# Performance work log

Measured on AMD Instinct MI355X. Metric: run time of the kernel, lower is better.

## Reference

```python
import jax, jax.numpy as jnp
import numpy as np

N_NODES = 4096
N_EDGES = 131072
F_DIM = 16
H_DIM = 32

def _mlp_params(key, in_dim, hidden):
    ks = jax.random.split(key, 6)
    s1 = 1.0 / np.sqrt(in_dim); s2 = 1.0 / np.sqrt(hidden)
    return dict(
        W1=jax.random.uniform(ks[0], (in_dim, hidden), jnp.float32, -s1, s1),
        b1=jax.random.uniform(ks[1], (hidden,), jnp.float32, -s1, s1),
        W2=jax.random.uniform(ks[2], (hidden, hidden), jnp.float32, -s2, s2),
        b2=jax.random.uniform(ks[3], (hidden,), jnp.float32, -s2, s2),
        W3=jax.random.uniform(ks[4], (hidden, 1), jnp.float32, -s2, s2),
        b3=jax.random.uniform(ks[5], (1,), jnp.float32, -s2, s2),
    )

def _mlp(x, W1, b1, W2, b2, W3, b3):
    h = jax.nn.relu(x @ W1 + b1)
    h = jax.nn.relu(h @ W2 + b2)
    return (h @ W3 + b3)[..., 0]  # (E,)

def setup_inputs() -> dict:
    key = jax.random.key(0)
    k_ei, k_ef, k_s, k_p = jax.random.split(key, 4)
    edge_index = jax.random.randint(k_ei, (N_EDGES, 2), 0, N_NODES, dtype=jnp.int32)
    edge_feat = jax.random.normal(k_ef, (N_EDGES, F_DIM), dtype=jnp.float32)
    sh = _mlp_params(k_s, F_DIM, H_DIM)
    sp = _mlp_params(k_p, F_DIM, H_DIM)
    return dict(
        species_idx=0,
        edge_index=edge_index,
        edge_feat=edge_feat,
        num_nodes=N_NODES,
        sW1=sh['W1'], sb1=sh['b1'], sW2=sh['W2'], sb2=sh['b2'], sW3=sh['W3'], sb3=sh['b3'],
        pW1=sp['W1'], pb1=sp['b1'], pW2=sp['W2'], pb2=sp['b2'], pW3=sp['W3'], pb3=sp['b3'],
    )

def reference(species_idx, edge_index, edge_feat, num_nodes,
              sW1, sb1, sW2, sb2, sW3, sb3,
              pW1, pb1, pW2, pb2, pW3, pb3):
    # Edge logits: shared head + species head (species_idx selects the head;
    # here the selected head's params are passed directly).
    shared = _mlp(edge_feat, sW1, sb1, sW2, sb2, sW3, sb3)   # (E,)
    species = _mlp(edge_feat, pW1, pb1, pW2, pb2, pW3, pb3)  # (E,)
    resistance = jax.nn.softplus(shared + species) + 1e-4
    conductance = 1.0 / resistance
    i = edge_index[:, 0]
    j = edge_index[:, 1]
    # Scatter-assembled graph Laplacian (N x N)
    L = jnp.zeros((num_nodes, num_nodes), dtype=edge_feat.dtype)
    L = L.at[i, i].add(conductance)
    L = L.at[j, j].add(conductance)
    L = L.at[i, j].add(-conductance)
    L = L.at[j, i].add(-conductance)
    L_pinv = jnp.linalg.pinv(L)
    diag = jnp.diagonal(L_pinv)
    R = diag[:, None] + diag[None, :] - 2.0 * L_pinv
    return R, shared, species
```

## Files before the change

kernel.cpp:

```cpp
#include <hip/hip_runtime.h>
#include <hip/hip_bf16.h>


#define NN 4096
#define LDA 4096
#define NEDGE 131072
#define INVN (1.0f/4096.0f)

__device__ __forceinline__ float mlp_eval(const float* __restrict__ w,
                                          const float* __restrict__ x) {
  float h1[32], h2[32];
#pragma unroll
  for (int o = 0; o < 32; o += 4) {
    float4 s = *(const float4*)&w[512 + o];
#pragma unroll
    for (int i = 0; i < 16; ++i) {
      float4 wv = *(const float4*)&w[i * 32 + o];
      s.x = fmaf(x[i], wv.x, s.x); s.y = fmaf(x[i], wv.y, s.y);
      s.z = fmaf(x[i], wv.z, s.z); s.w = fmaf(x[i], wv.w, s.w);
    }
    h1[o] = fmaxf(s.x, 0.f); h1[o+1] = fmaxf(s.y, 0.f);
    h1[o+2] = fmaxf(s.z, 0.f); h1[o+3] = fmaxf(s.w, 0.f);
  }
#pragma unroll
  for (int o = 0; o < 32; o += 4) {
    float4 s = *(const float4*)&w[1568 + o];
#pragma unroll
    for (int i = 0; i < 32; ++i) {
      float4 wv = *(const float4*)&w[544 + i * 32 + o];
      s.x = fmaf(h1[i], wv.x, s.x); s.y = fmaf(h1[i], wv.y, s.y);
      s.z = fmaf(h1[i], wv.z, s.z); s.w = fmaf(h1[i], wv.w, s.w);
    }
    h2[o] = fmaxf(s.x, 0.f); h2[o+1] = fmaxf(s.y, 0.f);
    h2[o+2] = fmaxf(s.z, 0.f); h2[o+3] = fmaxf(s.w, 0.f);
  }
  float out = w[1632];
#pragma unroll
  for (int i = 0; i < 32; ++i) out = fmaf(h2[i], w[1600 + i], out);
  return out;
}

__global__ __launch_bounds__(256) void mlp_kernel(
    const float* __restrict__ ef,
    const float* __restrict__ sW1, const float* __restrict__ sb1,
    const float* __restrict__ sW2, const float* __restrict__ sb2,
    const float* __restrict__ sW3, const float* __restrict__ sb3,
    const float* __restrict__ pW1, const float* __restrict__ pb1,
    const float* __restrict__ pW2, const float* __restrict__ pb2,
    const float* __restrict__ pW3, const float* __restrict__ pb3,
    float* __restrict__ outS, float* __restrict__ outP,
    float* __restrict__ cond) {
  __shared__ float w[3328];
  int t = threadIdx.x;
  for (int i = t; i < 512; i += 256) { w[i] = sW1[i]; w[1664 + i] = pW1[i]; }
  for (int i = t; i < 1024; i += 256) { w[544 + i] = sW2[i]; w[1664 + 544 + i] = pW2[i]; }
  if (t < 32) {
    w[512 + t] = sb1[t]; w[1568 + t] = sb2[t]; w[1600 + t] = sW3[t];
    w[1664 + 512 + t] = pb1[t]; w[1664 + 1568 + t] = pb2[t]; w[1664 + 1600 + t] = pW3[t];
  }
  if (t == 0) { w[1632] = sb3[0]; w[1664 + 1632] = pb3[0]; }
  __syncthreads();
  int e = blockIdx.x * 256 + t;
  float x[16];
#pragma unroll
  for (int i = 0; i < 16; i += 4) {
    float4 v = *(const float4*)&ef[(size_t)e * 16 + i];
    x[i] = v.x; x[i+1] = v.y; x[i+2] = v.z; x[i+3] = v.w;
  }
  float s = mlp_eval(w, x);
  float p = mlp_eval(w + 1664, x);
  outS[e] = s; outP[e] = p;
  float z = s + p;
  float sp = fmaxf(z, 0.f) + log1pf(expf(-fabsf(z)));
  cond[e] = 1.0f / (sp + 1e-4f);
}

__global__ __launch_bounds__(256) void init_A(float* __restrict__ A) {
  size_t q = (size_t)blockIdx.x * 256 + threadIdx.x;
  *(float4*)&A[q * 4] = make_float4(INVN, INVN, INVN, INVN);
}

__global__ __launch_bounds__(256) void scatter_kernel(const int* __restrict__ ei,
                                                      const float* __restrict__ cond,
                                                      float* __restrict__ A) {
  int e = blockIdx.x * 256 + threadIdx.x;
  int i = ei[2 * e], j = ei[2 * e + 1];
  float c = cond[e];
  atomicAdd(&A[(size_t)i * (LDA + 1)], c);
  atomicAdd(&A[(size_t)j * (LDA + 1)], c);
  atomicAdd(&A[(size_t)i * LDA + j], -c);
  atomicAdd(&A[(size_t)j * LDA + i], -c);
}

__device__ __forceinline__ float rlane(float v, int l) {
  return __int_as_float(__builtin_amdgcn_readlane(__float_as_int(v), l));
}

__global__ __launch_bounds__(64) void potf2_wave(float* __restrict__ A, int k,
                                                 float* __restrict__ GinvAll) {
  float* blk = A + (size_t)k * 64 * (LDA + 1);
  const int lane = threadIdx.x;
  float a[64], x[64];
#pragma unroll
  for (int c = 0; c < 64; c += 4) {
    float4 v = *(const float4*)&blk[(size_t)lane * LDA + c];
    a[c] = v.x; a[c+1] = v.y; a[c+2] = v.z; a[c+3] = v.w;
    x[c]   = (c   == lane) ? 1.f : 0.f;
    x[c+1] = (c+1 == lane) ? 1.f : 0.f;
    x[c+2] = (c+2 == lane) ? 1.f : 0.f;
    x[c+3] = (c+3 == lane) ? 1.f : 0.f;
  }
#pragma unroll
  for (int j = 0; j < 64; ++j) {
    float dj = rlane(a[j], j);
    float inv = 1.0f / sqrtf(dj);
    float lij = a[j] * inv;
    a[j] = lij;
    float coefT = -lij;
    float sX = (lane == j) ? inv : 1.0f;
    float coefX = (lane > j) ? -lij : 0.0f;
#pragma unroll
    for (int c = j + 1; c < 64; ++c)
      a[c] = fmaf(coefT, rlane(lij, c), a[c]);
#pragma unroll
    for (int c = 0; c <= j; ++c) {
      float xjc = rlane(x[c], j) * inv;
      x[c] = fmaf(coefX, xjc, x[c] * sX);
    }
  }
  float* Gk = GinvAll + (size_t)k * 4096;
#pragma unroll
  for (int c = 0; c < 64; c += 4) {
    *(float4*)&blk[(size_t)lane * LDA + c] = make_float4(a[c], a[c+1], a[c+2], a[c+3]);
    *(float4*)&Gk[lane * 64 + c] = make_float4(x[c], x[c+1], x[c+2], x[c+3]);
  }
}

template <bool TA, bool TB, bool ACCUM, bool LOWER, bool KST, bool CCOMP>
__global__ __launch_bounds__(256) void gemm64(
    const float* __restrict__ Ab, long long aZ, int lda,
    const float* __restrict__ Bb, long long bZ, int ldb,
    float* __restrict__ Cb, long long cZ, int ldc, int K, float alpha) {
  int ti = blockIdx.x, tj = blockIdx.y;
  if (LOWER && tj > ti) return;
  const float* A = Ab + (long long)blockIdx.z * aZ;
  const float* B = Bb + (long long)blockIdx.z * bZ;
  __shared__ float As[16][68], Bs[16][68];
  int tid = threadIdx.x;
  int tx = tid & 15, ty = tid >> 4;
  float acc[4][4] = {};
  int m0 = ti * 64, n0 = tj * 64;
  int k0 = KST ? ti * 64 : 0;
  for (int k = k0; k < K; k += 16) {
    if (!TA) {
      int r = tid >> 2, c4 = (tid & 3) * 4;
      float4 v = *(const float4*)&A[(size_t)(m0 + r) * lda + k + c4];
      As[c4 + 0][r] = v.x; As[c4 + 1][r] = v.y; As[c4 + 2][r] = v.z; As[c4 + 3][r] = v.w;
    } else {
      int r = tid >> 4, c4 = (tid & 15) * 4;
      *(float4*)&As[r][c4] = *(const float4*)&A[(size_t)(k + r) * lda + m0 + c4];
    }
    if (TB) {
      int r = tid >> 2, c4 = (tid & 3) * 4;
      float4 v = *(const float4*)&B[(size_t)(n0 + r) * ldb + k + c4];
      Bs[c4 + 0][r] = v.x; Bs[c4 + 1][r] = v.y; Bs[c4 + 2][r] = v.z; Bs[c4 + 3][r] = v.w;
    } else {
      int r = tid >> 4, c4 = (tid & 15) * 4;
      *(float4*)&Bs[r][c4] = *(const float4*)&B[(size_t)(k + r) * ldb + n0 + c4];
    }
    __syncthreads();
#pragma unroll
    for (int kk = 0; kk < 16; ++kk) {
      float4 av = *(const float4*)&As[kk][ty * 4];
      float4 bv = *(const float4*)&Bs[kk][tx * 4];
      float a[4] = {av.x, av.y, av.z, av.w};
      float b[4] = {bv.x, bv.y, bv.z, bv.w};
#pragma unroll
      for (int i = 0; i < 4; ++i)
#pragma unroll
        for (int jj = 0; jj < 4; ++jj) acc[i][jj] = fmaf(a[i], b[jj], acc[i][jj]);
    }
    __syncthreads();
  }
  if (CCOMP) {
    float* C = Cb + ((size_t)ti * (ti + 1) / 2 + tj) * 4096;
#pragma unroll
    for (int i = 0; i < 4; ++i) {
      float4 c;
      c.x = alpha * acc[i][0]; c.y = alpha * acc[i][1];
      c.z = alpha * acc[i][2]; c.w = alpha * acc[i][3];
      *(float4*)&C[(ty * 4 + i) * 64 + tx * 4] = c;
    }
  } else {
    float* C = Cb + (long long)blockIdx.z * cZ;
#pragma unroll
    for (int i = 0; i < 4; ++i) {
      size_t off = (size_t)(m0 + ty * 4 + i) * ldc + n0 + tx * 4;
      float4 c;
      if (ACCUM) {
        c = *(float4*)&C[off];
        c.x += alpha * acc[i][0]; c.y += alpha * acc[i][1];
        c.z += alpha * acc[i][2]; c.w += alpha * acc[i][3];
      } else {
        c.x = alpha * acc[i][0]; c.y = alpha * acc[i][1];
        c.z = alpha * acc[i][2]; c.w = alpha * acc[i][3];
      }
      *(float4*)&C[off] = c;
    }
  }
}

template <bool TA, bool LOWER, bool KST, bool CCOMP>
__global__ __launch_bounds__(256) void gemm128(
    const float* __restrict__ Ab, long long aZ, int lda,
    const float* __restrict__ Bb, long long bZ, int ldb,
    float* __restrict__ Cb, long long cZ, int ldc, int K, float alpha) {
  int ti = blockIdx.x, tj = blockIdx.y;
  if (LOWER && tj > ti) return;
  const float* A = Ab + (long long)blockIdx.z * aZ;
  const float* B = Bb + (long long)blockIdx.z * bZ;
  __shared__ float As[16][132], Bs[16][132];
  int tid = threadIdx.x;
  int tx = tid & 15, ty = tid >> 4;
  float acc[8][8] = {};
  int m0 = ti * 128, n0 = tj * 128;
  int k0 = KST ? ti * 128 : 0;
  for (int k = k0; k < K; k += 16) {
    if (!TA) {
      int r = tid >> 1, c8 = (tid & 1) * 8;
      const float* src = &A[(size_t)(m0 + r) * lda + k + c8];
      float4 v0 = *(const float4*)src;
      float4 v1 = *(const float4*)(src + 4);
      As[c8 + 0][r] = v0.x; As[c8 + 1][r] = v0.y; As[c8 + 2][r] = v0.z; As[c8 + 3][r] = v0.w;
      As[c8 + 4][r] = v1.x; As[c8 + 5][r] = v1.y; As[c8 + 6][r] = v1.z; As[c8 + 7][r] = v1.w;
    } else {
      int r = tid >> 4, c8 = (tid & 15) * 8;
      const float* src = &A[(size_t)(k + r) * lda + m0 + c8];
      *(float4*)&As[r][c8]     = *(const float4*)src;
      *(float4*)&As[r][c8 + 4] = *(const float4*)(src + 4);
    }
    {
      int r = tid >> 4, c8 = (tid & 15) * 8;
      const float* src = &B[(size_t)(k + r) * ldb + n0 + c8];
      *(float4*)&Bs[r][c8]     = *(const float4*)src;
      *(float4*)&Bs[r][c8 + 4] = *(const float4*)(src + 4);
    }
    __syncthreads();
#pragma unroll
    for (int kk = 0; kk < 16; ++kk) {
      float a8[8], b8[8];
      *(float4*)&a8[0] = *(const float4*)&As[kk][ty * 8];
      *(float4*)&a8[4] = *(const float4*)&As[kk][ty * 8 + 4];
      *(float4*)&b8[0] = *(const float4*)&Bs[kk][tx * 8];
      *(float4*)&b8[4] = *(const float4*)&Bs[kk][tx * 8 + 4];
#pragma unroll
      for (int i = 0; i < 8; ++i)
#pragma unroll
        for (int jj = 0; jj < 8; ++jj) acc[i][jj] = fmaf(a8[i], b8[jj], acc[i][jj]);
    }
    __syncthreads();
  }
  if (CCOMP) {
    int TI = 2 * ti + (ty >> 3), TJ = 2 * tj + (tx >> 3);
    if (TJ <= TI) {
      float* C = Cb + ((size_t)TI * (TI + 1) / 2 + TJ) * 4096;
      int rr = (ty & 7) * 8, cc = (tx & 7) * 8;
#pragma unroll
      for (int i = 0; i < 8; ++i) {
        float4 c0, c1;
        c0.x = alpha * acc[i][0]; c0.y = alpha * acc[i][1];
        c0.z = alpha * acc[i][2]; c0.w = alpha * acc[i][3];
        c1.x = alpha * acc[i][4]; c1.y = alpha * acc[i][5];
        c1.z = alpha * acc[i][6]; c1.w = alpha * acc[i][7];
        *(float4*)&C[(rr + i) * 64 + cc]     = c0;
        *(float4*)&C[(rr + i) * 64 + cc + 4] = c1;
      }
    }
  } else {
    float* C = Cb + (long long)blockIdx.z * cZ;
#pragma unroll
    for (int i = 0; i < 8; ++i) {
      float* dst = &C[(size_t)(m0 + ty * 8 + i) * ldc + n0 + tx * 8];
      float4 c0, c1;
      c0.x = alpha * acc[i][0]; c0.y = alpha * acc[i][1];
      c0.z = alpha * acc[i][2]; c0.w = alpha * acc[i][3];
      c1.x = alpha * acc[i][4]; c1.y = alpha * acc[i][5];
      c1.z = alpha * acc[i][6]; c1.w = alpha * acc[i][7];
      *(float4*)dst       = c0;
      *(float4*)(dst + 4) = c1;
    }
  }
}

__global__ __launch_bounds__(256) void finish_W_prep(float* __restrict__ A,
                                                     const float* __restrict__ GinvAll) {
  size_t q = (size_t)blockIdx.x * 256 + threadIdx.x;
  int r = (int)(q >> 10), c4 = (int)(q & 1023) << 2;
  int rb = r >> 6, cb = c4 >> 6;
  if (cb == rb) {
    const float* g = GinvAll + (size_t)rb * 4096 + (size_t)(r & 63) * 64 + (c4 & 63);
    *(float4*)&A[q * 4] = *(const float4*)g;
  } else if (cb > rb) {
    *(float4*)&A[q * 4] = make_float4(0.f, 0.f, 0.f, 0.f);
  }
}

__global__ __launch_bounds__(256) void copy_diag(const float* __restrict__ Mc,
                                                 float* __restrict__ d) {
  int i = blockIdx.x * 256 + threadIdx.x;
  int tb = i >> 6;
  size_t q = (size_t)tb * (tb + 1) / 2 + tb;
  d[i] = Mc[q * 4096 + (size_t)(i & 63) * 65];
}

__global__ __launch_bounds__(256) void final_R(const float* __restrict__ Mc,
                                               const float* __restrict__ d,
                                               float* __restrict__ out) {
  size_t idx = (size_t)blockIdx.x * 256 + threadIdx.x;
  int r = (int)(idx >> 12), c = (int)(idx & 4095);
  int a = r > c ? r : c, b = r > c ? c : r;
  int ta = a >> 6, tb = b >> 6;
  size_t q = (size_t)ta * (ta + 1) / 2 + tb;
  float m = Mc[q * 4096 + (size_t)(a & 63) * 64 + (b & 63)];
  out[idx] = d[r] + d[c] - 2.0f * m;
}

extern "C" void kernel_launch(void* const* d_in, const int* in_sizes, int n_in,
                              void* d_out, int out_size, void* d_ws, size_t ws_size,
                              hipStream_t stream) {
  const int* eidx = (const int*)d_in[1];
  const float* ef = (const float*)d_in[2];
  const float* sW1 = (const float*)d_in[4],  *sb1 = (const float*)d_in[5];
  const float* sW2 = (const float*)d_in[6],  *sb2 = (const float*)d_in[7];
  const float* sW3 = (const float*)d_in[8],  *sb3 = (const float*)d_in[9];
  const float* pW1 = (const float*)d_in[10], *pb1 = (const float*)d_in[11];
  const float* pW2 = (const float*)d_in[12], *pb2 = (const float*)d_in[13];
  const float* pW3 = (const float*)d_in[14], *pb3 = (const float*)d_in[15];

  float* dout = (float*)d_out;
  float* dA = dout;
  float* outS = dout + (size_t)NN * NN;
  float* outP = outS + NEDGE;

  float* ws = (float*)d_ws;
  float* Mc = ws;
  float* U = ws + 8519680ull;
  float* cond = U;
  float* Ginv = U;
  float* Tbuf = U;
  float* diagb = U;

  mlp_kernel<<<NEDGE / 256, 256, 0, stream>>>(ef, sW1, sb1, sW2, sb2, sW3, sb3,
                                              pW1, pb1, pW2, pb2, pW3, pb3,
                                              outS, outP, cond);
  init_A<<<(NN * NN / 4) / 256, 256, 0, stream>>>(dA);
  scatter_kernel<<<NEDGE / 256, 256, 0, stream>>>(eidx, cond, dA);

  for (int k = 0; k < NN / 64; ++k) {
    potf2_wave<<<1, 64, 0, stream>>>(dA, k, Ginv);
    int rem = NN - (k + 1) * 64;
    if (rem > 0) {
      float* panel = dA + (size_t)(k + 1) * 64 * LDA + (size_t)k * 64;
      gemm64<false, true, false, false, false, false>
          <<<dim3(rem / 64, 1, 1), 256, 0, stream>>>(
              panel, 0, LDA, Ginv + (size_t)k * 4096, 0, 64, panel, 0, LDA, 64, 1.0f);
      float* trail = dA + (size_t)(k + 1) * 64 * (LDA + 1);
      gemm64<false, true, true, true, false, false>
          <<<dim3(rem / 64, rem / 64, 1), 256, 0, stream>>>(
              panel, 0, LDA, panel, 0, LDA, trail, 0, LDA, 64, -1.0f);
    }
  }

  finish_W_prep<<<(NN * NN / 4) / 256, 256, 0, stream>>>(dA, Ginv);

  for (int S = 64; S <= 2048; S *= 2) {
    int np = NN / (2 * S);
    long long pz = (long long)2 * S * (LDA + 1);
    if (S == 64) {
      gemm64<false, false, false, false, false, false>
          <<<dim3(1, 1, np), 256, 0, stream>>>(
              dA + (size_t)S * LDA, pz, LDA, dA, pz, LDA,
              Tbuf, (long long)S * S, S, S, 1.0f);
      gemm64<false, false, false, false, false, false>
          <<<dim3(1, 1, np), 256, 0, stream>>>(
              dA + (size_t)S * (LDA + 1), pz, LDA, Tbuf, (long long)S * S, S,
              dA + (size_t)S * LDA, pz, LDA, S, -1.0f);
    } else {
      gemm128<false, false, false, false>
          <<<dim3(S / 128, S / 128, np), 256, 0, stream>>>(
              dA + (size_t)S * LDA, pz, LDA, dA, pz, LDA,
              Tbuf, (long long)S * S, S, S, 1.0f);
      gemm128<false, false, false, false>
          <<<dim3(S / 128, S / 128, np), 256, 0, stream>>>(
              dA + (size_t)S * (LDA + 1), pz, LDA, Tbuf, (long long)S * S, S,
              dA + (size_t)S * LDA, pz, LDA, S, -1.0f);
    }
  }

  gemm128<true, true, true, true>
      <<<dim3(32, 32, 1), 256, 0, stream>>>(dA, 0, LDA, dA, 0, LDA, Mc, 0, 64,
                                            NN, 1.0f);

  copy_diag<<<NN / 256, 256, 0, stream>>>(Mc, diagb);
  final_R<<<(NN * NN) / 256, 256, 0, stream>>>(Mc, diagb, dout);
}
```

Measured before the change: 5.160 ms.

## Block Cholesky into 256-wide panels with large 128-tile trailing SYRK updates

```diff
diff --git a/kernel.cpp b/kernel.cpp
--- a/kernel.cpp
+++ b/kernel.cpp
@@ -210,13 +210,21 @@
   }
 }
 
-template <bool TA, bool LOWER, bool KST, bool CCOMP>
+template <bool TA, bool TB, bool ACCUM, bool TRI, bool KST, bool CCOMP>
 __global__ __launch_bounds__(256) void gemm128(
     const float* __restrict__ Ab, long long aZ, int lda,
     const float* __restrict__ Bb, long long bZ, int ldb,
     float* __restrict__ Cb, long long cZ, int ldc, int K, float alpha) {
-  int ti = blockIdx.x, tj = blockIdx.y;
-  if (LOWER && tj > ti) return;
+  int ti, tj;
+  if (TRI) {
+    int bid = blockIdx.x;
+    ti = (int)((sqrtf(8.0f * bid + 1.0f) - 1.0f) * 0.5f);
+    while ((ti + 1) * (ti + 2) / 2 <= bid) ++ti;
+    while (ti * (ti + 1) / 2 > bid) --ti;
+    tj = bid - ti * (ti + 1) / 2;
+  } else {
+    ti = blockIdx.x; tj = blockIdx.y;
+  }
   const float* A = Ab + (long long)blockIdx.z * aZ;
   const float* B = Bb + (long long)blockIdx.z * bZ;
   __shared__ float As[16][132], Bs[16][132];
@@ -239,7 +247,14 @@
       *(float4*)&As[r][c8]     = *(const float4*)src;
       *(float4*)&As[r][c8 + 4] = *(const float4*)(src + 4);
     }
-    {
+    if (TB) {
+      int r = tid >> 1, c8 = (tid & 1) * 8;
+      const float* src = &B[(size_t)(n0 + r) * ldb + k + c8];
+      float4 v0 = *(const float4*)src;
+      float4 v1 = *(const float4*)(src + 4);
+      Bs[c8 + 0][r] = v0.x; Bs[c8 + 1][r] = v0.y; Bs[c8 + 2][r] = v0.z; Bs[c8 + 3][r] = v0.w;
+      Bs[c8 + 4][r] = v1.x; Bs[c8 + 5][r] = v1.y; Bs[c8 + 6][r] = v1.z; Bs[c8 + 7][r] = v1.w;
+    } else {
       int r = tid >> 4, c8 = (tid & 15) * 8;
       const float* src = &B[(size_t)(k + r) * ldb + n0 + c8];
       *(float4*)&Bs[r][c8]     = *(const float4*)src;
@@ -249,10 +264,10 @@
 #pragma unroll
     for (int kk = 0; kk < 16; ++kk) {
       float a8[8], b8[8];
-      *(float4*)&a8[0] = *(const float4*)&As[kk][ty * 8];
-      *(float4*)&a8[4] = *(const float4*)&As[kk][ty * 8 + 4];
-      *(float4*)&b8[0] = *(const float4*)&Bs[kk][tx * 8];
-      *(float4*)&b8[4] = *(const float4*)&Bs[kk][tx * 8 + 4];
+      *(float4*)&a8[0] = *(const float4*)&As[kk][ty * 4];
+      *(float4*)&a8[4] = *(const float4*)&As[kk][64 + ty * 4];
+      *(float4*)&b8[0] = *(const float4*)&Bs[kk][tx * 4];
+      *(float4*)&b8[4] = *(const float4*)&Bs[kk][64 + tx * 4];
 #pragma unroll
       for (int i = 0; i < 8; ++i)
 #pragma unroll
@@ -261,33 +276,44 @@
     __syncthreads();
   }
   if (CCOMP) {
-    int TI = 2 * ti + (ty >> 3), TJ = 2 * tj + (tx >> 3);
-    if (TJ <= TI) {
-      float* C = Cb + ((size_t)TI * (TI + 1) / 2 + TJ) * 4096;
-      int rr = (ty & 7) * 8, cc = (tx & 7) * 8;
-#pragma unroll
-      for (int i = 0; i < 8; ++i) {
-        float4 c0, c1;
-        c0.x = alpha * acc[i][0]; c0.y = alpha * acc[i][1];
-        c0.z = alpha * acc[i][2]; c0.w = alpha * acc[i][3];
-        c1.x = alpha * acc[i][4]; c1.y = alpha * acc[i][5];
-        c1.z = alpha * acc[i][6]; c1.w = alpha * acc[i][7];
-        *(float4*)&C[(rr + i) * 64 + cc]     = c0;
-        *(float4*)&C[(rr + i) * 64 + cc + 4] = c1;
+#pragma unroll
+    for (int hr = 0; hr < 2; ++hr) {
+      int TI = 2 * ti + hr;
+#pragma unroll
+      for (int hc = 0; hc < 2; ++hc) {
+        int TJ = 2 * tj + hc;
+        if (TJ > TI) continue;
+        float* C = Cb + ((size_t)TI * (TI + 1) / 2 + TJ) * 4096;
+#pragma unroll
+        for (int i = 0; i < 4; ++i) {
+          float4 c;
+          c.x = alpha * acc[hr * 4 + i][hc * 4 + 0];
+          c.y = alpha * acc[hr * 4 + i][hc * 4 + 1];
+          c.z = alpha * acc[hr * 4 + i][hc * 4 + 2];
+          c.w = alpha * acc[hr * 4 + i][hc * 4 + 3];
+          *(float4*)&C[(ty * 4 + i) * 64 + tx * 4] = c;
+        }
       }
     }
   } else {
     float* C = Cb + (long long)blockIdx.z * cZ;
 #pragma unroll
     for (int i = 0; i < 8; ++i) {
-      float* dst = &C[(size_t)(m0 + ty * 8 + i) * ldc + n0 + tx * 8];
+      int row = (i < 4) ? (m0 + ty * 4 + i) : (m0 + 64 + ty * 4 + i - 4);
+      float* dst0 = &C[(size_t)row * ldc + n0 + tx * 4];
+      float* dst1 = dst0 + 64;
       float4 c0, c1;
       c0.x = alpha * acc[i][0]; c0.y = alpha * acc[i][1];
       c0.z = alpha * acc[i][2]; c0.w = alpha * acc[i][3];
       c1.x = alpha * acc[i][4]; c1.y = alpha * acc[i][5];
       c1.z = alpha * acc[i][6]; c1.w = alpha * acc[i][7];
-      *(float4*)dst       = c0;
-      *(float4*)(dst + 4) = c1;
+      if (ACCUM) {
+        float4 o0 = *(float4*)dst0, o1 = *(float4*)dst1;
+        c0.x += o0.x; c0.y += o0.y; c0.z += o0.z; c0.w += o0.w;
+        c1.x += o1.x; c1.y += o1.y; c1.z += o1.z; c1.w += o1.w;
+      }
+      *(float4*)dst0 = c0;
+      *(float4*)dst1 = c1;
     }
   }
 }
@@ -356,18 +382,36 @@
   init_A<<<(NN * NN / 4) / 256, 256, 0, stream>>>(dA);
   scatter_kernel<<<NEDGE / 256, 256, 0, stream>>>(eidx, cond, dA);
 
-  for (int k = 0; k < NN / 64; ++k) {
-    potf2_wave<<<1, 64, 0, stream>>>(dA, k, Ginv);
-    int rem = NN - (k + 1) * 64;
-    if (rem > 0) {
-      float* panel = dA + (size_t)(k + 1) * 64 * LDA + (size_t)k * 64;
-      gemm64<false, true, false, false, false, false>
-          <<<dim3(rem / 64, 1, 1), 256, 0, stream>>>(
-              panel, 0, LDA, Ginv + (size_t)k * 4096, 0, 64, panel, 0, LDA, 64, 1.0f);
-      float* trail = dA + (size_t)(k + 1) * 64 * (LDA + 1);
-      gemm64<false, true, true, true, false, false>
-          <<<dim3(rem / 64, rem / 64, 1), 256, 0, stream>>>(
-              panel, 0, LDA, panel, 0, LDA, trail, 0, LDA, 64, -1.0f);
+  for (int p = 0; p < 16; ++p) {
+    int ct = p * 4;
+    for (int kk = 0; kk < 4; ++kk) {
+      int k = ct + kk;
+      potf2_wave<<<1, 64, 0, stream>>>(dA, k, Ginv);
+      int rem = NN - (k + 1) * 64;
+      if (rem > 0) {
+        float* panel = dA + (size_t)(k + 1) * 64 * LDA + (size_t)k * 64;
+        gemm64<false, true, false, false, false, false>
+            <<<dim3(rem / 64, 1, 1), 256, 0, stream>>>(
+                panel, 0, LDA, Ginv + (size_t)k * 4096, 0, 64, panel, 0, LDA,
+                64, 1.0f);
+        int pcols = 3 - kk;
+        if (pcols > 0) {
+          float* trail = dA + (size_t)(k + 1) * 64 * (LDA + 1);
+          gemm64<false, true, true, true, false, false>
+              <<<dim3(rem / 64, pcols, 1), 256, 0, stream>>>(
+                  panel, 0, LDA, panel, 0, LDA, trail, 0, LDA, 64, -1.0f);
+        }
+      }
+    }
+    int c0 = p * 256;
+    int rem2 = NN - c0 - 256;
+    if (rem2 > 0) {
+      float* Lp = dA + (size_t)(c0 + 256) * LDA + c0;
+      float* trail = dA + (size_t)(c0 + 256) * (LDA + 1);
+      int nt = rem2 / 128;
+      gemm128<false, true, true, true, false, false>
+          <<<dim3(nt * (nt + 1) / 2, 1, 1), 256, 0, stream>>>(
+              Lp, 0, LDA, Lp, 0, LDA, trail, 0, LDA, 256, -1.0f);
     }
   }
 
@@ -386,19 +430,19 @@
               dA + (size_t)S * (LDA + 1), pz, LDA, Tbuf, (long long)S * S, S,
               dA + (size_t)S * LDA, pz, LDA, S, -1.0f);
     } else {
-      gemm128<false, false, false, false>
+      gemm128<false, false, false, false, false, false>
           <<<dim3(S / 128, S / 128, np), 256, 0, stream>>>(
               dA + (size_t)S * LDA, pz, LDA, dA, pz, LDA,
               Tbuf, (long long)S * S, S, S, 1.0f);
-      gemm128<false, false, false, false>
+      gemm128<false, false, false, false, false, false>
           <<<dim3(S / 128, S / 128, np), 256, 0, stream>>>(
               dA + (size_t)S * (LDA + 1), pz, LDA, Tbuf, (long long)S * S, S,
               dA + (size_t)S * LDA, pz, LDA, S, -1.0f);
     }
   }
 
-  gemm128<true, true, true, true>
-      <<<dim3(32, 32, 1), 256, 0, stream>>>(dA, 0, LDA, dA, 0, LDA, Mc, 0, 64,
+  gemm128<true, false, false, true, true, true>
+      <<<dim3(528, 1, 1), 256, 0, stream>>>(dA, 0, LDA, dA, 0, LDA, Mc, 0, 64,
                                             NN, 1.0f);
 
   copy_diag<<<NN / 256, 256, 0, stream>>>(Mc, diagb);
```

Measured after the change: 5.171 ms. No clear change (+0.2%).
